# Optimization experiments

Hardware: AMD Instinct MI355X
Metric: run time of the kernel (lower is better)

The kernel has to match this reference:

```python
import jax, jax.numpy as jnp
import numpy as np
import math

D_MODEL = 1024
NHEAD = 16
HEAD_DIM = D_MODEL // NHEAD
SCALE = math.sqrt(HEAD_DIM)
B, TQ, TK = 8, 1024, 1024


def setup_inputs() -> dict:
    key = jax.random.key(0)
    ks = jax.random.split(key, 8)
    init = 0.02
    return {
        "query": jax.random.normal(ks[0], (B, TQ, D_MODEL), jnp.float32),
        "memory": jax.random.normal(ks[1], (B, TK, D_MODEL), jnp.float32),
        "coverage": jax.random.uniform(ks[2], (B, TK), jnp.float32),
        "Wq": jax.random.normal(ks[3], (D_MODEL, D_MODEL), jnp.float32) * init,
        "bq": jnp.zeros((D_MODEL,), jnp.float32),
        "Wk": jax.random.normal(ks[4], (D_MODEL, D_MODEL), jnp.float32) * init,
        "bk": jnp.zeros((D_MODEL,), jnp.float32),
        "Wv": jax.random.normal(ks[5], (D_MODEL, D_MODEL), jnp.float32) * init,
        "bv": jnp.zeros((D_MODEL,), jnp.float32),
        "Wo": jax.random.normal(ks[6], (D_MODEL, D_MODEL), jnp.float32) * init,
        "bo": jnp.zeros((D_MODEL,), jnp.float32),
        "Wcov": jax.random.normal(ks[7], (NHEAD, 1), jnp.float32) * init,
    }


def reference(query, memory, coverage, Wq, bq, Wk, bk, Wv, bv, Wo, bo, Wcov):
    b, tq, _ = query.shape
    tk = memory.shape[1]
    # projections, split into heads: [B, H, T, hd]
    Q = (query @ Wq.T + bq).reshape(b, tq, NHEAD, HEAD_DIM).transpose(0, 2, 1, 3)
    K = (memory @ Wk.T + bk).reshape(b, tk, NHEAD, HEAD_DIM).transpose(0, 2, 1, 3)
    V = (memory @ Wv.T + bv).reshape(b, tk, NHEAD, HEAD_DIM).transpose(0, 2, 1, 3)
    scores = jnp.einsum('bhqd,bhkd->bhqk', Q, K) / SCALE
    # coverage_proj: Linear(1, nhead, bias=False) -> outer product coverage x Wcov[:,0]
    cov_bias = jnp.einsum('bk,h->bhk', coverage, Wcov[:, 0])[:, :, None, :]  # [B,H,1,Tk]
    scores = scores + cov_bias
    attn = jax.nn.softmax(scores, axis=-1)
    # dropout is identity in eval/deterministic mode
    out = jnp.einsum('bhqk,bhkd->bhqd', attn, V).transpose(0, 2, 1, 3).reshape(b, tq, D_MODEL)
    out = out @ Wo.T + bo
    new_coverage = coverage + attn.mean(axis=1).sum(axis=1)  # [B,Tk]
    return out, new_coverage
```

## Files before the change

kernel.cpp:

```cpp
#include <hip/hip_runtime.h>

typedef __bf16 bf16_t;
typedef bf16_t bf16x8 __attribute__((ext_vector_type(8)));
typedef float f32x4 __attribute__((ext_vector_type(4)));

#define MFMA16(a, b, c) __builtin_amdgcn_mfma_f32_16x16x32_bf16(a, b, c, 0, 0, 0)

#define LOG2E 1.44269504f
#define C1 0.18033688f

#define WAIT_VM4_LGKM0 0x074
#define WAIT_VM2_LGKM0 0x072
#define WAIT_VM0_LGKM0 0x070

__device__ inline void barrier_ws() {
  __asm__ volatile("" ::: "memory");
  __builtin_amdgcn_s_barrier();
  __asm__ volatile("" ::: "memory");
}

__device__ inline void async_copy16(const bf16_t* g, bf16_t* l) {
  __builtin_amdgcn_global_load_lds(
      (const __attribute__((address_space(1))) void*)g,
      (__attribute__((address_space(3))) void*)l, 16, 0, 0);
}

__device__ inline bf16x8 lds_frag(const bf16_t* lds, int row, int c8) {
  return *(const bf16x8*)(lds + row * 64 + ((c8 ^ (row & 7)) << 3));
}

template <int NCHUNK, int NT>
__device__ inline void stage_tile(const bf16_t* __restrict__ g, size_t ld,
                                  bf16_t* lds, int tid) {
#pragma unroll
  for (int it = 0; it < NCHUNK / NT; ++it) {
    int f = it * NT + tid;
    int row = f >> 3;
    int c8 = (f & 7) ^ (row & 7);
    async_copy16(g + (size_t)row * ld + c8 * 8, lds + f * 8);
  }
}

__global__ __launch_bounds__(256) void convert_kernel(
    const float* __restrict__ q, const float* __restrict__ mem,
    const float* __restrict__ wq, const float* __restrict__ wk,
    const float* __restrict__ wv, const float* __restrict__ wo,
    const float* __restrict__ coverage, bf16_t* Xq, bf16_t* Xm, bf16_t* Wqb,
    bf16_t* Wkb, bf16_t* Wvb, bf16_t* Wob, float* covout) {
  size_t i = ((size_t)blockIdx.x * 256 + threadIdx.x) * 8;
  if (i >= 20971520u) {
    size_t off = i - 20971520u;
    *(float4*)(covout + off) = *(const float4*)(coverage + off);
    *(float4*)(covout + off + 4) = *(const float4*)(coverage + off + 4);
    return;
  }
  const float* src;
  bf16_t* dst;
  size_t off;
  if (i < 8388608u)        { src = q;   dst = Xq;  off = i; }
  else if (i < 16777216u)  { src = mem; dst = Xm;  off = i - 8388608u; }
  else if (i < 17825792u)  { src = wq;  dst = Wqb; off = i - 16777216u; }
  else if (i < 18874368u)  { src = wk;  dst = Wkb; off = i - 17825792u; }
  else if (i < 19922944u)  { src = wv;  dst = Wvb; off = i - 18874368u; }
  else                     { src = wo;  dst = Wob; off = i - 19922944u; }
  float4 f0 = *(const float4*)(src + off);
  float4 f1 = *(const float4*)(src + off + 4);
  union { bf16_t h[8]; uint4 u; } t;
  t.h[0] = (bf16_t)f0.x; t.h[1] = (bf16_t)f0.y;
  t.h[2] = (bf16_t)f0.z; t.h[3] = (bf16_t)f0.w;
  t.h[4] = (bf16_t)f1.x; t.h[5] = (bf16_t)f1.y;
  t.h[6] = (bf16_t)f1.z; t.h[7] = (bf16_t)f1.w;
  *(uint4*)(dst + off) = t.u;
}

__global__ __launch_bounds__(256) void gemm_qkv(
    const bf16_t* __restrict__ Xq, const bf16_t* __restrict__ Xm,
    const bf16_t* __restrict__ Wqkv, const float* __restrict__ bq,
    const float* __restrict__ bk, const float* __restrict__ bv,
    bf16_t* __restrict__ Qp, bf16_t* __restrict__ Kp,
    bf16_t* __restrict__ Vt) {
  __shared__ bf16_t As[128 * 64];
  __shared__ bf16_t Bs[128 * 64];
  const int tid = threadIdx.x;
  const int wave = tid >> 6, lane = tid & 63, quad = lane >> 4, c = lane & 15;
  const int wm = (wave & 1) * 64, wn = (wave >> 1) * 64;
  const size_t bm = blockIdx.x, bn = blockIdx.y;
  const int which = (int)(bn >> 3);
  const bf16_t* A = which ? Xm : Xq;
  const float* bias = which == 0 ? bq : (which == 1 ? bk : bv);
  const bf16_t* Ab = A + bm * 128 * 1024;
  const bf16_t* Bb = Wqkv + bn * 128 * 1024;
  const f32x4 z4 = {0.f, 0.f, 0.f, 0.f};
  f32x4 acc[4][4];
#pragma unroll
  for (int i = 0; i < 4; ++i)
#pragma unroll
    for (int j = 0; j < 4; ++j) acc[i][j] = z4;

  for (int kt = 0; kt < 16; ++kt) {
    if (kt) __syncthreads();
    stage_tile<1024, 256>(Ab + kt * 64, 1024, As, tid);
    stage_tile<1024, 256>(Bb + kt * 64, 1024, Bs, tid);
    __syncthreads();
#pragma unroll
    for (int ks = 0; ks < 2; ++ks) {
      bf16x8 af[4], bfr[4];
#pragma unroll
      for (int i = 0; i < 4; ++i)
        af[i] = lds_frag(As, wm + 16 * i + c, ks * 4 + quad);
#pragma unroll
      for (int j = 0; j < 4; ++j)
        bfr[j] = lds_frag(Bs, wn + 16 * j + c, ks * 4 + quad);
#pragma unroll
      for (int i = 0; i < 4; ++i)
#pragma unroll
        for (int j = 0; j < 4; ++j)
          acc[i][j] = MFMA16(af[i], bfr[j], acc[i][j]);
    }
  }
#pragma unroll
  for (int i = 0; i < 4; ++i)
#pragma unroll
    for (int j = 0; j < 4; ++j) {
      int gc = (int)bn * 128 + wn + 16 * j + c;
      int gcl = gc & 1023;
      float bvv = bias[gcl];
      if (which == 2) {
        int b = (int)(bm >> 3);
        int kk = (int)(bm & 7) * 128 + wm + 16 * i + quad * 4;
        union { bf16_t h4[4]; uint2 u; } pk;
#pragma unroll
        for (int r = 0; r < 4; ++r) pk.h4[r] = (bf16_t)(acc[i][j][r] + bvv);
        *(uint2*)(Vt + ((size_t)(b * 1024 + gcl)) * 1024 + kk) = pk.u;
      } else {
        bf16_t* Cout = which ? Kp : Qp;
        int gr0 = (int)bm * 128 + wm + 16 * i + quad * 4;
#pragma unroll
        for (int r = 0; r < 4; ++r)
          Cout[(size_t)(gr0 + r) * 1024 + gcl] = (bf16_t)(acc[i][j][r] + bvv);
      }
    }
}

__global__ __launch_bounds__(256) void gemm_out(
    const bf16_t* __restrict__ A, const bf16_t* __restrict__ Bw,
    const float* __restrict__ bias, float* __restrict__ Cout) {
  __shared__ bf16_t As[128 * 64];
  __shared__ bf16_t Bs[128 * 64];
  const int tid = threadIdx.x;
  const int wave = tid >> 6, lane = tid & 63, quad = lane >> 4, c = lane & 15;
  const int wm = (wave & 1) * 64, wn = (wave >> 1) * 64;
  const size_t bm = blockIdx.x, bn = blockIdx.y;
  const bf16_t* Ab = A + bm * 128 * 1024;
  const bf16_t* Bb = Bw + bn * 128 * 1024;
  const f32x4 z4 = {0.f, 0.f, 0.f, 0.f};
  f32x4 acc[4][4];
#pragma unroll
  for (int i = 0; i < 4; ++i)
#pragma unroll
    for (int j = 0; j < 4; ++j) acc[i][j] = z4;

  for (int kt = 0; kt < 16; ++kt) {
    if (kt) __syncthreads();
    stage_tile<1024, 256>(Ab + kt * 64, 1024, As, tid);
    stage_tile<1024, 256>(Bb + kt * 64, 1024, Bs, tid);
    __syncthreads();
#pragma unroll
    for (int ks = 0; ks < 2; ++ks) {
      bf16x8 af[4], bfr[4];
#pragma unroll
      for (int i = 0; i < 4; ++i)
        af[i] = lds_frag(As, wm + 16 * i + c, ks * 4 + quad);
#pragma unroll
      for (int j = 0; j < 4; ++j)
        bfr[j] = lds_frag(Bs, wn + 16 * j + c, ks * 4 + quad);
#pragma unroll
      for (int i = 0; i < 4; ++i)
#pragma unroll
        for (int j = 0; j < 4; ++j)
          acc[i][j] = MFMA16(af[i], bfr[j], acc[i][j]);
    }
  }
#pragma unroll
  for (int i = 0; i < 4; ++i)
#pragma unroll
    for (int j = 0; j < 4; ++j) {
      int gc = (int)bn * 128 + wn + 16 * j + c;
      float bvv = bias[gc];
      int gr0 = (int)bm * 128 + wm + 16 * i + quad * 4;
#pragma unroll
      for (int r = 0; r < 4; ++r)
        Cout[(size_t)(gr0 + r) * 1024 + gc] = acc[i][j][r] + bvv;
    }
}

__global__ __launch_bounds__(256) void attn_fwd(
    const bf16_t* __restrict__ Qp, const bf16_t* __restrict__ Kp,
    const bf16_t* __restrict__ Vt, const float* __restrict__ coverage,
    const float* __restrict__ Wcov, bf16_t* __restrict__ Hb,
    float* __restrict__ linvG) {
  __shared__ bf16_t Qs[64 * 64];
  __shared__ bf16_t Ks[2][64 * 64];
  __shared__ bf16_t Vs[2][64 * 64];
  __shared__ bf16_t Ps[4][16 * 64];
  __shared__ float covb[1024];
  const int tid = threadIdx.x;
  const int wave = tid >> 6, lane = tid & 63, quad = lane >> 4, c = lane & 15;
  const int q0 = blockIdx.x * 64, h = blockIdx.y, b = blockIdx.z;
  const float wcl = Wcov[h] * LOG2E;
  const f32x4 z4 = {0.f, 0.f, 0.f, 0.f};
  const bf16_t* Kbase = Kp + ((size_t)b * 1024) * 1024 + h * 64;
  const bf16_t* Vbase = Vt + ((size_t)(b * 1024 + h * 64)) * 1024;

  stage_tile<512, 256>(Qp + ((size_t)(b * 1024 + q0)) * 1024 + h * 64, 1024,
                       Qs, tid);
  for (int i = tid; i < 1024; i += 256) covb[i] = coverage[b * 1024 + i] * wcl;
  stage_tile<512, 256>(Kbase, 1024, Ks[0], tid);
  stage_tile<512, 256>(Vbase, 1024, Vs[0], tid);

  f32x4 O[4] = {z4, z4, z4, z4};
  f32x4 Ol = z4;
  bf16x8 qf0, qf1;
  union { bf16_t h8[8]; bf16x8 v; } ones;
#pragma unroll
  for (int t = 0; t < 8; ++t) ones.h8[t] = (bf16_t)1.0f;
  bf16_t* Pw = &Ps[wave][0];

  auto tile_step = [&](int kt, const bf16_t* curK, const bf16_t* curV,
                       bf16_t* nxtK, bf16_t* nxtV) {
    if (kt < 15) {
      stage_tile<512, 256>(Kbase + (size_t)(kt + 1) * 64 * 1024, 1024, nxtK,
                           tid);
      stage_tile<512, 256>(Vbase + (kt + 1) * 64, 1024, nxtV, tid);
      __builtin_amdgcn_s_waitcnt(WAIT_VM4_LGKM0);
    } else {
      __builtin_amdgcn_s_waitcnt(WAIT_VM0_LGKM0);
    }
    barrier_ws();
    if (kt == 0) {
      qf0 = lds_frag(Qs, wave * 16 + c, quad);
      qf1 = lds_frag(Qs, wave * 16 + c, 4 + quad);
    }
    const int k0 = kt * 64;
    f32x4 S[4] = {z4, z4, z4, z4};
#pragma unroll
    for (int j = 0; j < 4; ++j) {
      S[j] = MFMA16(lds_frag(curK, j * 16 + c, quad), qf0, S[j]);
      S[j] = MFMA16(lds_frag(curK, j * 16 + c, 4 + quad), qf1, S[j]);
    }
#pragma unroll
    for (int j = 0; j < 4; ++j) {
      f32x4 cb = *(const f32x4*)&covb[k0 + j * 16 + quad * 4];
      union { bf16_t h4[4]; uint2 u; } pk;
#pragma unroll
      for (int r = 0; r < 4; ++r)
        pk.h4[r] = (bf16_t)exp2f(S[j][r] * C1 + cb[r]);
      int k8 = j * 2 + (quad >> 1);
      *(uint2*)(Pw + c * 64 + ((k8 ^ (c & 7)) << 3) + (quad & 1) * 4) = pk.u;
    }
#pragma unroll
    for (int ks = 0; ks < 2; ++ks) {
      bf16x8 pb =
          *(const bf16x8*)(Pw + c * 64 + (((ks * 4 + quad) ^ (c & 7)) << 3));
#pragma unroll
      for (int j = 0; j < 4; ++j)
        O[j] = MFMA16(lds_frag(curV, j * 16 + c, ks * 4 + quad), pb, O[j]);
      Ol = MFMA16(ones.v, pb, Ol);
    }
    barrier_ws();
  };

#pragma unroll 1
  for (int kt2 = 0; kt2 < 16; kt2 += 2) {
    tile_step(kt2, Ks[0], Vs[0], Ks[1], Vs[1]);
    tile_step(kt2 + 1, Ks[1], Vs[1], Ks[0], Vs[0]);
  }

  float linv = 1.f / Ol[0];
  if (quad == 0)
    linvG[((size_t)(b * 16 + h)) * 1024 + q0 + wave * 16 + c] = linv;

  size_t rowbase = ((size_t)(b * 1024 + q0 + wave * 16 + c)) * 1024 + h * 64;
#pragma unroll
  for (int j = 0; j < 4; ++j) {
    union { bf16_t h4[4]; uint2 u; } pk;
#pragma unroll
    for (int r = 0; r < 4; ++r) pk.h4[r] = (bf16_t)(O[j][r] * linv);
    *(uint2*)(Hb + rowbase + j * 16 + quad * 4) = pk.u;
  }
}

__global__ __launch_bounds__(256) void cov_kernel(
    const bf16_t* __restrict__ Qp, const bf16_t* __restrict__ Kp,
    const float* __restrict__ coverage, const float* __restrict__ Wcov,
    const float* __restrict__ linvG, float* __restrict__ covout) {
  __shared__ bf16_t Ks[64 * 64];
  __shared__ bf16_t Qs[2][64 * 64];
  __shared__ float covsum[64];
  const int tid = threadIdx.x;
  const int wave = tid >> 6, lane = tid & 63, quad = lane >> 4, c = lane & 15;
  const int k0 = blockIdx.x * 64, h = blockIdx.y, b = blockIdx.z;
  const float wcl = Wcov[h] * LOG2E;
  const f32x4 z4 = {0.f, 0.f, 0.f, 0.f};
  const bf16_t* Qbase = Qp + ((size_t)b * 1024) * 1024 + h * 64;
  const float* lbase = linvG + ((size_t)(b * 16 + h)) * 1024 + wave * 16 + c;

  f32x4 cbv[4];
#pragma unroll
  for (int j = 0; j < 4; ++j) {
    cbv[j] = *(const f32x4*)&coverage[b * 1024 + k0 + j * 16 + quad * 4];
#pragma unroll
    for (int r = 0; r < 4; ++r) cbv[j][r] *= wcl;
  }
  float lv_cur = lbase[0];

  if (tid < 64) covsum[tid] = 0.f;
  stage_tile<512, 256>(Kp + ((size_t)(b * 1024 + k0)) * 1024 + h * 64, 1024,
                       Ks, tid);
  stage_tile<512, 256>(Qbase, 1024, Qs[0], tid);

  float cs[4][4] = {};
  bf16x8 kf0[4], kf1[4];

  auto q_step = [&](int qt, const bf16_t* curQ, bf16_t* nxtQ) {
    float lv_nxt = 0.f;
    if (qt < 15) {
      lv_nxt = lbase[(qt + 1) * 64];
      stage_tile<512, 256>(Qbase + (size_t)(qt + 1) * 64 * 1024, 1024, nxtQ,
                           tid);
      __builtin_amdgcn_s_waitcnt(WAIT_VM2_LGKM0);
    } else {
      __builtin_amdgcn_s_waitcnt(WAIT_VM0_LGKM0);
    }
    barrier_ws();
    if (qt == 0) {
#pragma unroll
      for (int j = 0; j < 4; ++j) {
        kf0[j] = lds_frag(Ks, j * 16 + c, quad);
        kf1[j] = lds_frag(Ks, j * 16 + c, 4 + quad);
      }
    }
    bf16x8 qa = lds_frag(curQ, wave * 16 + c, quad);
    bf16x8 qb = lds_frag(curQ, wave * 16 + c, 4 + quad);
    f32x4 S[4] = {z4, z4, z4, z4};
#pragma unroll
    for (int j = 0; j < 4; ++j) {
      S[j] = MFMA16(kf0[j], qa, S[j]);
      S[j] = MFMA16(kf1[j], qb, S[j]);
    }
#pragma unroll
    for (int j = 0; j < 4; ++j)
#pragma unroll
      for (int r = 0; r < 4; ++r)
        cs[j][r] += exp2f(S[j][r] * C1 + cbv[j][r]) * lv_cur;
    lv_cur = lv_nxt;
    barrier_ws();
  };

#pragma unroll 1
  for (int qt2 = 0; qt2 < 16; qt2 += 2) {
    q_step(qt2, Qs[0], Qs[1]);
    q_step(qt2 + 1, Qs[1], Qs[0]);
  }

#pragma unroll
  for (int j = 0; j < 4; ++j)
#pragma unroll
    for (int r = 0; r < 4; ++r) {
      float v = cs[j][r];
      v += __shfl_xor(v, 1);
      v += __shfl_xor(v, 2);
      v += __shfl_xor(v, 4);
      v += __shfl_xor(v, 8);
      if (c == 0) atomicAdd(&covsum[j * 16 + quad * 4 + r], v);
    }
  __syncthreads();
  if (tid < 64)
    atomicAdd(&covout[b * 1024 + k0 + tid], covsum[tid] * 0.0625f);
}

extern "C" void kernel_launch(void* const* d_in, const int* in_sizes, int n_in,
                              void* d_out, int out_size, void* d_ws,
                              size_t ws_size, hipStream_t stream) {
  const float* query = (const float*)d_in[0];
  const float* memory = (const float*)d_in[1];
  const float* coverage = (const float*)d_in[2];
  const float* Wq = (const float*)d_in[3];
  const float* bq = (const float*)d_in[4];
  const float* Wk = (const float*)d_in[5];
  const float* bk = (const float*)d_in[6];
  const float* Wv = (const float*)d_in[7];
  const float* bv = (const float*)d_in[8];
  const float* Wo = (const float*)d_in[9];
  const float* bo = (const float*)d_in[10];
  const float* Wcov = (const float*)d_in[11];

  char* w = (char*)d_ws;
  const size_t MB = 1024 * 1024;
  bf16_t* Xq = (bf16_t*)(w + 0);
  bf16_t* Xm = (bf16_t*)(w + 16 * MB);
  bf16_t* Wqb = (bf16_t*)(w + 32 * MB);
  bf16_t* Wkb = (bf16_t*)(w + 34 * MB);
  bf16_t* Wvb = (bf16_t*)(w + 36 * MB);
  bf16_t* Wob = (bf16_t*)(w + 38 * MB);
  bf16_t* Qp = (bf16_t*)(w + 40 * MB);
  bf16_t* Kp = (bf16_t*)(w + 56 * MB);
  bf16_t* Vt = (bf16_t*)(w + 72 * MB);
  bf16_t* Hb = (bf16_t*)(w + 0);
  float* linvG = (float*)(w + 16 * MB);

  float* out = (float*)d_out;
  float* covout = out + (size_t)8 * 1024 * 1024;

  convert_kernel<<<10244, 256, 0, stream>>>(query, memory, Wq, Wk, Wv, Wo,
                                            coverage, Xq, Xm, Wqb, Wkb, Wvb,
                                            Wob, covout);
  gemm_qkv<<<dim3(64, 24), 256, 0, stream>>>(Xq, Xm, Wqb, bq, bk, bv, Qp, Kp,
                                             Vt);
  attn_fwd<<<dim3(16, 16, 8), 256, 0, stream>>>(Qp, Kp, Vt, coverage, Wcov,
                                                Hb, linvG);
  cov_kernel<<<dim3(16, 16, 8), 256, 0, stream>>>(Qp, Kp, coverage, Wcov,
                                                  linvG, covout);
  gemm_out<<<dim3(64, 8), 256, 0, stream>>>(Hb, Wob, bo, out);
}
```

Before: 346.2 us.

## Fold coverage bias into V and softmax scale into Q, single-buffer attention

```diff
diff --git a/kernel.cpp b/kernel.cpp
--- a/kernel.cpp
+++ b/kernel.cpp
@@ -45,9 +45,26 @@
     const float* __restrict__ q, const float* __restrict__ mem,
     const float* __restrict__ wq, const float* __restrict__ wk,
     const float* __restrict__ wv, const float* __restrict__ wo,
-    const float* __restrict__ coverage, bf16_t* Xq, bf16_t* Xm, bf16_t* Wqb,
-    bf16_t* Wkb, bf16_t* Wvb, bf16_t* Wob, float* covout) {
+    const float* __restrict__ coverage, const float* __restrict__ Wcov,
+    bf16_t* Xq, bf16_t* Xm, bf16_t* Wqb, bf16_t* Wkb, bf16_t* Wvb,
+    bf16_t* Wob, float* covout, bf16_t* covE) {
   size_t i = ((size_t)blockIdx.x * 256 + threadIdx.x) * 8;
+  if (i >= 20979712u) {
+    size_t off = i - 20979712u;
+    int k = (int)(off & 1023);
+    int bh = (int)(off >> 10);
+    int b = bh >> 4, h = bh & 15;
+    float w = Wcov[h] * LOG2E;
+    float4 c0 = *(const float4*)(coverage + (b << 10) + k);
+    float4 c1 = *(const float4*)(coverage + (b << 10) + k + 4);
+    union { bf16_t h8[8]; uint4 u; } t;
+    t.h8[0] = (bf16_t)exp2f(c0.x * w); t.h8[1] = (bf16_t)exp2f(c0.y * w);
+    t.h8[2] = (bf16_t)exp2f(c0.z * w); t.h8[3] = (bf16_t)exp2f(c0.w * w);
+    t.h8[4] = (bf16_t)exp2f(c1.x * w); t.h8[5] = (bf16_t)exp2f(c1.y * w);
+    t.h8[6] = (bf16_t)exp2f(c1.z * w); t.h8[7] = (bf16_t)exp2f(c1.w * w);
+    *(uint4*)(covE + off) = t.u;
+    return;
+  }
   if (i >= 20971520u) {
     size_t off = i - 20971520u;
     *(float4*)(covout + off) = *(const float4*)(coverage + off);
@@ -77,8 +94,8 @@
     const bf16_t* __restrict__ Xq, const bf16_t* __restrict__ Xm,
     const bf16_t* __restrict__ Wqkv, const float* __restrict__ bq,
     const float* __restrict__ bk, const float* __restrict__ bv,
-    bf16_t* __restrict__ Qp, bf16_t* __restrict__ Kp,
-    bf16_t* __restrict__ Vt) {
+    const bf16_t* __restrict__ covE, bf16_t* __restrict__ Qp,
+    bf16_t* __restrict__ Kp, bf16_t* __restrict__ Vt) {
   __shared__ bf16_t As[128 * 64];
   __shared__ bf16_t Bs[128 * 64];
   const int tid = threadIdx.x;
@@ -127,17 +144,23 @@
       float bvv = bias[gcl];
       if (which == 2) {
         int b = (int)(bm >> 3);
+        int hh = gcl >> 6;
         int kk = (int)(bm & 7) * 128 + wm + 16 * i + quad * 4;
+        union { bf16_t h4[4]; uint2 u; } ev;
+        ev.u = *(const uint2*)(covE + ((size_t)(b * 16 + hh)) * 1024 + kk);
         union { bf16_t h4[4]; uint2 u; } pk;
 #pragma unroll
-        for (int r = 0; r < 4; ++r) pk.h4[r] = (bf16_t)(acc[i][j][r] + bvv);
+        for (int r = 0; r < 4; ++r)
+          pk.h4[r] = (bf16_t)((acc[i][j][r] + bvv) * (float)ev.h4[r]);
         *(uint2*)(Vt + ((size_t)(b * 1024 + gcl)) * 1024 + kk) = pk.u;
       } else {
         bf16_t* Cout = which ? Kp : Qp;
+        float scale = which ? 1.0f : C1;
         int gr0 = (int)bm * 128 + wm + 16 * i + quad * 4;
 #pragma unroll
         for (int r = 0; r < 4; ++r)
-          Cout[(size_t)(gr0 + r) * 1024 + gcl] = (bf16_t)(acc[i][j][r] + bvv);
+          Cout[(size_t)(gr0 + r) * 1024 + gcl] =
+              (bf16_t)((acc[i][j][r] + bvv) * scale);
       }
     }
 }
@@ -194,67 +217,55 @@
     }
 }
 
-__global__ __launch_bounds__(256) void attn_fwd(
+__global__ __launch_bounds__(256, 6) void attn_fwd(
     const bf16_t* __restrict__ Qp, const bf16_t* __restrict__ Kp,
-    const bf16_t* __restrict__ Vt, const float* __restrict__ coverage,
-    const float* __restrict__ Wcov, bf16_t* __restrict__ Hb,
-    float* __restrict__ linvG) {
-  __shared__ bf16_t Qs[64 * 64];
-  __shared__ bf16_t Ks[2][64 * 64];
-  __shared__ bf16_t Vs[2][64 * 64];
-  __shared__ bf16_t Ps[4][16 * 64];
-  __shared__ float covb[1024];
+    const bf16_t* __restrict__ Vt, const bf16_t* __restrict__ covE,
+    bf16_t* __restrict__ Hb, float* __restrict__ linvG) {
+  __shared__ bf16_t QPs[64 * 64];
+  __shared__ bf16_t Ks[64 * 64];
+  __shared__ bf16_t Vs[64 * 64];
+  __shared__ bf16_t Es[1024];
   const int tid = threadIdx.x;
   const int wave = tid >> 6, lane = tid & 63, quad = lane >> 4, c = lane & 15;
   const int q0 = blockIdx.x * 64, h = blockIdx.y, b = blockIdx.z;
-  const float wcl = Wcov[h] * LOG2E;
   const f32x4 z4 = {0.f, 0.f, 0.f, 0.f};
   const bf16_t* Kbase = Kp + ((size_t)b * 1024) * 1024 + h * 64;
   const bf16_t* Vbase = Vt + ((size_t)(b * 1024 + h * 64)) * 1024;
 
   stage_tile<512, 256>(Qp + ((size_t)(b * 1024 + q0)) * 1024 + h * 64, 1024,
-                       Qs, tid);
-  for (int i = tid; i < 1024; i += 256) covb[i] = coverage[b * 1024 + i] * wcl;
-  stage_tile<512, 256>(Kbase, 1024, Ks[0], tid);
-  stage_tile<512, 256>(Vbase, 1024, Vs[0], tid);
+                       QPs, tid);
+  if (tid < 128)
+    async_copy16(covE + ((size_t)(b * 16 + h)) * 1024 + tid * 8,
+                 Es + tid * 8);
+  stage_tile<512, 256>(Kbase, 1024, Ks, tid);
+  stage_tile<512, 256>(Vbase, 1024, Vs, tid);
+  __builtin_amdgcn_s_waitcnt(WAIT_VM4_LGKM0);
+  barrier_ws();
+  bf16x8 qf0 = lds_frag(QPs, wave * 16 + c, quad);
+  bf16x8 qf1 = lds_frag(QPs, wave * 16 + c, 4 + quad);
+  bf16_t* Pw = &QPs[wave * 16 * 64];
 
   f32x4 O[4] = {z4, z4, z4, z4};
   f32x4 Ol = z4;
-  bf16x8 qf0, qf1;
-  union { bf16_t h8[8]; bf16x8 v; } ones;
-#pragma unroll
-  for (int t = 0; t < 8; ++t) ones.h8[t] = (bf16_t)1.0f;
-  bf16_t* Pw = &Ps[wave][0];
-
-  auto tile_step = [&](int kt, const bf16_t* curK, const bf16_t* curV,
-                       bf16_t* nxtK, bf16_t* nxtV) {
-    if (kt < 15) {
-      stage_tile<512, 256>(Kbase + (size_t)(kt + 1) * 64 * 1024, 1024, nxtK,
-                           tid);
-      stage_tile<512, 256>(Vbase + (kt + 1) * 64, 1024, nxtV, tid);
-      __builtin_amdgcn_s_waitcnt(WAIT_VM4_LGKM0);
-    } else {
-      __builtin_amdgcn_s_waitcnt(WAIT_VM0_LGKM0);
-    }
-    barrier_ws();
-    if (kt == 0) {
-      qf0 = lds_frag(Qs, wave * 16 + c, quad);
-      qf1 = lds_frag(Qs, wave * 16 + c, 4 + quad);
-    }
-    const int k0 = kt * 64;
+
+  for (int kt = 0; kt < 16; ++kt) {
+    if (kt) {
+      __syncthreads();
+      stage_tile<512, 256>(Kbase + (size_t)kt * 64 * 1024, 1024, Ks, tid);
+      stage_tile<512, 256>(Vbase + kt * 64, 1024, Vs, tid);
+    }
+    __syncthreads();
     f32x4 S[4] = {z4, z4, z4, z4};
 #pragma unroll
     for (int j = 0; j < 4; ++j) {
-      S[j] = MFMA16(lds_frag(curK, j * 16 + c, quad), qf0, S[j]);
-      S[j] = MFMA16(lds_frag(curK, j * 16 + c, 4 + quad), qf1, S[j]);
+      S[j] = MFMA16(lds_frag(Ks, j * 16 + c, quad), qf0, S[j]);
+      S[j] = MFMA16(lds_frag(Ks, j * 16 + c, 4 + quad), qf1, S[j]);
     }
 #pragma unroll
     for (int j = 0; j < 4; ++j) {
-      f32x4 cb = *(const f32x4*)&covb[k0 + j * 16 + quad * 4];
       union { bf16_t h4[4]; uint2 u; } pk;
 #pragma unroll
-      for (int r = 0; r < 4; ++r)
-        pk.h4[r] = (bf16_t)exp2f(S[j][r] * C1 + cb[r]);
+      for (int r = 0; r < 4; ++r) pk.h4[r] = (bf16_t)exp2f(S[j][r]);
       int k8 = j * 2 + (quad >> 1);
       *(uint2*)(Pw + c * 64 + ((k8 ^ (c & 7)) << 3) + (quad & 1) * 4) = pk.u;
     }
@@ -262,18 +273,12 @@
     for (int ks = 0; ks < 2; ++ks) {
       bf16x8 pb =
           *(const bf16x8*)(Pw + c * 64 + (((ks * 4 + quad) ^ (c & 7)) << 3));
+      bf16x8 ef = *(const bf16x8*)(Es + kt * 64 + ks * 32 + quad * 8);
 #pragma unroll
       for (int j = 0; j < 4; ++j)
-        O[j] = MFMA16(lds_frag(curV, j * 16 + c, ks * 4 + quad), pb, O[j]);
-      Ol = MFMA16(ones.v, pb, Ol);
-    }
-    barrier_ws();
-  };
-
-#pragma unroll 1
-  for (int kt2 = 0; kt2 < 16; kt2 += 2) {
-    tile_step(kt2, Ks[0], Vs[0], Ks[1], Vs[1]);
-    tile_step(kt2 + 1, Ks[1], Vs[1], Ks[0], Vs[0]);
+        O[j] = MFMA16(lds_frag(Vs, j * 16 + c, ks * 4 + quad), pb, O[j]);
+      Ol = MFMA16(ef, pb, Ol);
+    }
   }
 
   float linv = 1.f / Ol[0];
@@ -290,28 +295,19 @@
   }
 }
 
-__global__ __launch_bounds__(256) void cov_kernel(
+__global__ __launch_bounds__(256, 4) void cov_kernel(
     const bf16_t* __restrict__ Qp, const bf16_t* __restrict__ Kp,
-    const float* __restrict__ coverage, const float* __restrict__ Wcov,
-    const float* __restrict__ linvG, float* __restrict__ covout) {
+    const bf16_t* __restrict__ covE, const float* __restrict__ linvG,
+    float* __restrict__ covout) {
   __shared__ bf16_t Ks[64 * 64];
   __shared__ bf16_t Qs[2][64 * 64];
   __shared__ float covsum[64];
   const int tid = threadIdx.x;
   const int wave = tid >> 6, lane = tid & 63, quad = lane >> 4, c = lane & 15;
   const int k0 = blockIdx.x * 64, h = blockIdx.y, b = blockIdx.z;
-  const float wcl = Wcov[h] * LOG2E;
   const f32x4 z4 = {0.f, 0.f, 0.f, 0.f};
   const bf16_t* Qbase = Qp + ((size_t)b * 1024) * 1024 + h * 64;
   const float* lbase = linvG + ((size_t)(b * 16 + h)) * 1024 + wave * 16 + c;
-
-  f32x4 cbv[4];
-#pragma unroll
-  for (int j = 0; j < 4; ++j) {
-    cbv[j] = *(const f32x4*)&coverage[b * 1024 + k0 + j * 16 + quad * 4];
-#pragma unroll
-    for (int r = 0; r < 4; ++r) cbv[j][r] *= wcl;
-  }
   float lv_cur = lbase[0];
 
   if (tid < 64) covsum[tid] = 0.f;
@@ -351,8 +347,7 @@
 #pragma unroll
     for (int j = 0; j < 4; ++j)
 #pragma unroll
-      for (int r = 0; r < 4; ++r)
-        cs[j][r] += exp2f(S[j][r] * C1 + cbv[j][r]) * lv_cur;
+      for (int r = 0; r < 4; ++r) cs[j][r] += exp2f(S[j][r]) * lv_cur;
     lv_cur = lv_nxt;
     barrier_ws();
   };
@@ -375,8 +370,10 @@
       if (c == 0) atomicAdd(&covsum[j * 16 + quad * 4 + r], v);
     }
   __syncthreads();
-  if (tid < 64)
-    atomicAdd(&covout[b * 1024 + k0 + tid], covsum[tid] * 0.0625f);
+  if (tid < 64) {
+    float e = (float)covE[((size_t)(b * 16 + h)) * 1024 + k0 + tid];
+    atomicAdd(&covout[b * 1024 + k0 + tid], covsum[tid] * e * 0.0625f);
+  }
 }
 
 extern "C" void kernel_launch(void* const* d_in, const int* in_sizes, int n_in,
@@ -406,20 +403,20 @@
   bf16_t* Qp = (bf16_t*)(w + 40 * MB);
   bf16_t* Kp = (bf16_t*)(w + 56 * MB);
   bf16_t* Vt = (bf16_t*)(w + 72 * MB);
+  bf16_t* covE = (bf16_t*)(w + 88 * MB);
   bf16_t* Hb = (bf16_t*)(w + 0);
   float* linvG = (float*)(w + 16 * MB);
 
   float* out = (float*)d_out;
   float* covout = out + (size_t)8 * 1024 * 1024;
 
-  convert_kernel<<<10244, 256, 0, stream>>>(query, memory, Wq, Wk, Wv, Wo,
-                                            coverage, Xq, Xm, Wqb, Wkb, Wvb,
-                                            Wob, covout);
-  gemm_qkv<<<dim3(64, 24), 256, 0, stream>>>(Xq, Xm, Wqb, bq, bk, bv, Qp, Kp,
-                                             Vt);
-  attn_fwd<<<dim3(16, 16, 8), 256, 0, stream>>>(Qp, Kp, Vt, coverage, Wcov,
-                                                Hb, linvG);
-  cov_kernel<<<dim3(16, 16, 8), 256, 0, stream>>>(Qp, Kp, coverage, Wcov,
-                                                  linvG, covout);
+  convert_kernel<<<10308, 256, 0, stream>>>(query, memory, Wq, Wk, Wv, Wo,
+                                            coverage, Wcov, Xq, Xm, Wqb, Wkb,
+                                            Wvb, Wob, covout, covE);
+  gemm_qkv<<<dim3(64, 24), 256, 0, stream>>>(Xq, Xm, Wqb, bq, bk, bv, covE,
+                                             Qp, Kp, Vt);
+  attn_fwd<<<dim3(16, 16, 8), 256, 0, stream>>>(Qp, Kp, Vt, covE, Hb, linvG);
+  cov_kernel<<<dim3(16, 16, 8), 256, 0, stream>>>(Qp, Kp, covE, linvG,
+                                                  covout);
   gemm_out<<<dim3(64, 8), 256, 0, stream>>>(Hb, Wob, bo, out);
 }
```

New measurement: 321.8 us. 7.0% less time.
